# Kernel optimization log

Hardware: AMD Instinct MI355X
Metric: run time of the kernel (lower is better)

Reference implementation:

```python
import jax, jax.numpy as jnp
import numpy as np

WIDTH = 4096
NUM_HEADS = 8
BLOCK_W = WIDTH // NUM_HEADS


def _block_diag_linear(x, w, b):
    # x: [n, width] -> [n, h, bw]; w: [h, bw, bw]; b: [h, bw]
    n = x.shape[0]
    xh = x.reshape(n, NUM_HEADS, BLOCK_W)
    y = jnp.einsum('nhi,hij->nhj', xh, w) + b
    return y.reshape(n, WIDTH)


def setup_inputs() -> dict:
    key = jax.random.key(0)
    ks = jax.random.split(key, 7)
    n = 8192
    x = jax.random.normal(ks[0], (n, WIDTH), dtype=jnp.float32)
    s = jnp.sort(jax.random.randint(ks[1], (n,), 0, 8, dtype=jnp.int32))
    # a_param init: uniform on ring radii [0.9, 0.999], softplus-inverse transform
    eps = 1e-8
    u = jax.random.uniform(ks[2], (WIDTH,), minval=0.9**2 + eps, maxval=0.999**2 + eps)
    t = 0.5 * jnp.log(u)
    a_param = jnp.log(jnp.exp(-t) - 1.0).astype(jnp.float32)
    std = 1.0 / np.sqrt(BLOCK_W)
    ig_w = std * jax.random.normal(ks[3], (NUM_HEADS, BLOCK_W, BLOCK_W), dtype=jnp.float32)
    ig_b = jnp.zeros((NUM_HEADS, BLOCK_W), dtype=jnp.float32)
    ag_w = std * jax.random.normal(ks[4], (NUM_HEADS, BLOCK_W, BLOCK_W), dtype=jnp.float32)
    ag_b = jnp.zeros((NUM_HEADS, BLOCK_W), dtype=jnp.float32)
    return {'x': x, 's': s, 'a_param': a_param, 'ig_w': ig_w, 'ig_b': ig_b,
            'ag_w': ag_w, 'ag_b': ag_b}


def reference(x, s, a_param, ig_w, ig_b, ag_w, ag_b):
    n, k = x.shape
    # reset mask: True at position 0 and wherever segment id changes
    reset = jnp.concatenate([jnp.ones((1,), dtype=bool), s[1:] != s[:-1]])
    gate_x = jax.nn.sigmoid(_block_diag_linear(x, ig_w, ig_b))
    gate_a = jax.nn.sigmoid(_block_diag_linear(x, ag_w, ag_b))
    log_a = -8.0 * gate_a * jax.nn.softplus(a_param)  # [n, k]
    a = jnp.exp(log_a)
    a_square = jnp.exp(2.0 * log_a)
    multiplier = jnp.sqrt(1.0 - a_square)
    multiplier = jnp.where(reset[:, None], 1.0, multiplier)
    normalized_x = x * gate_x * multiplier
    # linear recurrence h[t] = a[t] * h[t-1] + normalized_x[t] via parallel scan
    def combine(e1, e2):
        a1, b1 = e1
        a2, b2 = e2
        return (a1 * a2, a2 * b1 + b2)
    _, out = jax.lax.associative_scan(combine, (a, normalized_x), axis=0)
    return out
```

## Files before the change

kernel.cpp:

```cpp
#include <hip/hip_runtime.h>
#include <hip/hip_bf16.h>
#include <stdint.h>

#define WIDTH 4096
#define NROWS 8192
#define NHEADS 8
#define BW 512
#define CS 128
#define NCHUNK (NROWS/CS)

typedef short bf16x8 __attribute__((ext_vector_type(8)));
typedef float f32x4 __attribute__((ext_vector_type(4)));

__device__ __forceinline__ uint32_t rne_bf16(float f) {
  uint32_t u = __float_as_uint(f);
  return (u + 0x7fffu + ((u >> 16) & 1u)) >> 16;
}
__device__ __forceinline__ uint32_t pack2(float lo, float hi) {
  return rne_bf16(lo) | (rne_bf16(hi) << 16);
}
__device__ __forceinline__ float bf16_to_f32(uint32_t bits) {
  return __uint_as_float(bits << 16);
}

__device__ __forceinline__ void gload_lds16(const void* g, void* l) {
  __builtin_amdgcn_global_load_lds(
      (const __attribute__((address_space(1))) void*)g,
      (__attribute__((address_space(3))) void*)l, 16, 0, 0);
}

__global__ void prep_xbf16(const float* __restrict__ x, uint16_t* __restrict__ xb) {
  size_t i = ((size_t)blockIdx.x * 256 + threadIdx.x) * 8;
  float4 f0 = *reinterpret_cast<const float4*>(x + i);
  float4 f1 = *reinterpret_cast<const float4*>(x + i + 4);
  uint4 v;
  v.x = pack2(f0.x, f0.y); v.y = pack2(f0.z, f0.w);
  v.z = pack2(f1.x, f1.y); v.w = pack2(f1.z, f1.w);
  *reinterpret_cast<uint4*>(xb + i) = v;
}

__global__ void prep_weights(const float* __restrict__ ig_w,
                             const float* __restrict__ ag_w,
                             uint16_t* __restrict__ wt) {
  __shared__ float tile[32][33];
  int j0 = blockIdx.x * 32;
  int i0 = blockIdx.y * 32;
  int m  = blockIdx.z;
  const float* src = ((m >> 3) ? ag_w : ig_w) + (size_t)(m & 7) * BW * BW;
  int tx = threadIdx.x & 31, ty = threadIdx.x >> 5;
  #pragma unroll
  for (int k = 0; k < 4; k++) {
    int i = i0 + ty + 8 * k;
    tile[ty + 8 * k][tx] = src[(size_t)i * BW + (j0 + tx)];
  }
  __syncthreads();
  #pragma unroll
  for (int k = 0; k < 4; k++) {
    int j = j0 + ty + 8 * k;
    wt[((size_t)m * BW + j) * BW + (i0 + tx)] = (uint16_t)rne_bf16(tile[tx][ty + 8 * k]);
  }
}

__global__ void prep_misc(const float* __restrict__ a_param, float* __restrict__ cvec) {
  int i = blockIdx.x * 256 + threadIdx.x;
  if (i < WIDTH) {
    float x = a_param[i];
    float sp = (x > 15.f) ? x : log1pf(expf(x));
    cvec[i] = 8.f * sp;
  }
}

#define BM 128
#define BN 128
#define BK 64

__global__ __launch_bounds__(256, 2)
void gates_gemm(const uint16_t* __restrict__ xb,
                const int* __restrict__ s,
                const uint16_t* __restrict__ wt,
                const float* __restrict__ ig_b,
                const float* __restrict__ ag_b,
                const float* __restrict__ cvec,
                uint16_t* __restrict__ la_buf,
                uint16_t* __restrict__ nx_buf,
                float* __restrict__ cA,
                float* __restrict__ cB) {
  __shared__ __align__(16) unsigned char smem[49152];
  __shared__ unsigned char resetm[BM];

  const int b = blockIdx.x;
  const int orig = (b & 7) * 256 + (b >> 3);
  const int h  = orig >> 8;
  const int rem = orig & 255;
  const int mt = rem >> 2;
  const int nt = rem & 3;
  const int m0 = mt * BM;
  const int j0 = nt * BN;

  const int tid = threadIdx.x;
  const int lane = tid & 63;
  const int w = tid >> 6;
  const int wr = w >> 1;
  const int wc = w & 1;
  const int lrow = lane & 15;
  const int lkg  = lane >> 4;

  if (tid < BM) {
    int n = m0 + tid;
    resetm[tid] = (n == 0) || (s[n] != s[n - 1]);
  }

  const char* xb_src[4];
  #pragma unroll
  for (int i = 0; i < 4; i++) {
    int o = (4 * w + i) * 1024 + (lane << 4);
    int row = o >> 7;
    int c = (o & 127) ^ ((row & 7) << 4);
    xb_src[i] = (const char*)xb + ((size_t)(m0 + row) * WIDTH + h * BW) * 2 + c;
  }
  const char* w_src[8];
  #pragma unroll
  for (int i = 0; i < 8; i++) {
    int o = (8 * w + i) * 1024 + (lane << 4);
    int g = o >> 14;
    int jl = (o >> 7) & 127;
    int c = (o & 127) ^ ((jl & 7) << 4);
    w_src[i] = (const char*)wt + ((size_t)((g * 8 + h) * BW + (j0 + jl)) * BW) * 2 + c;
  }

  f32x4 acc[2][4][4];
  #pragma unroll
  for (int g = 0; g < 2; g++)
    #pragma unroll
    for (int mf = 0; mf < 4; mf++)
      #pragma unroll
      for (int nf = 0; nf < 4; nf++)
        acc[g][mf][nf] = (f32x4){0.f, 0.f, 0.f, 0.f};

  for (int kt = 0; kt < 8; kt++) {
    __syncthreads();
    #pragma unroll
    for (int i = 0; i < 4; i++)
      gload_lds16(xb_src[i] + kt * 128, smem + (4 * w + i) * 1024);
    #pragma unroll
    for (int i = 0; i < 8; i++)
      gload_lds16(w_src[i] + kt * 128, smem + 16384 + (8 * w + i) * 1024);
    __syncthreads();
    #pragma unroll
    for (int ks = 0; ks < 2; ks++) {
      bf16x8 af[4];
      #pragma unroll
      for (int mf = 0; mf < 4; mf++) {
        int row = wr * 64 + 16 * mf + lrow;
        uint32_t addr = (uint32_t)((row << 7) + ks * 64 + lkg * 16);
        addr ^= (uint32_t)((row & 7) << 4);
        af[mf] = *reinterpret_cast<const bf16x8*>(smem + addr);
      }
      #pragma unroll
      for (int g = 0; g < 2; g++) {
        #pragma unroll
        for (int nf = 0; nf < 4; nf++) {
          int j = wc * 64 + 16 * nf + lrow;
          uint32_t addr = (uint32_t)(16384 + (g << 14) + (j << 7) + ks * 64 + lkg * 16);
          addr ^= (uint32_t)((j & 7) << 4);
          bf16x8 bfr = *reinterpret_cast<const bf16x8*>(smem + addr);
          #pragma unroll
          for (int mf = 0; mf < 4; mf++) {
            acc[g][mf][nf] = __builtin_amdgcn_mfma_f32_16x16x32_bf16(
                af[mf], bfr, acc[g][mf][nf], 0, 0, 0);
          }
        }
      }
    }
  }

  __syncthreads();
  float* smf = (float*)smem;

  #pragma unroll
  for (int nf = 0; nf < 4; nf++) {
    int j = j0 + wc * 64 + 16 * nf + lrow;
    int jj = h * BW + j;
    float igb = ig_b[jj], agb = ag_b[jj], cv = cvec[jj];
    float segA[4], segB[4];
    #pragma unroll
    for (int mf = 0; mf < 4; mf++) {
      float A = 1.f, B = 0.f;
      int nbase = m0 + wr * 64 + 16 * mf + 4 * lkg;
      #pragma unroll
      for (int r = 0; r < 4; r++) {
        int n = nbase + r;
        size_t o = (size_t)n * WIDTH + jj;
        float yig = acc[0][mf][nf][r] + igb;
        float yag = acc[1][mf][nf][r] + agb;
        float gx = __builtin_amdgcn_rcpf(1.f + __expf(-yig));
        float ga = __builtin_amdgcn_rcpf(1.f + __expf(-yag));
        float la = -ga * cv;
        uint32_t la_bits = rne_bf16(la);
        float la_r = bf16_to_f32(la_bits);
        float a = __expf(la_r);
        float mult = resetm[n - m0] ? 1.f
                     : __builtin_amdgcn_sqrtf(fmaxf(1.f - a * a, 0.f));
        float xv = bf16_to_f32((uint32_t)xb[o]);
        float nx = xv * gx * mult;
        uint32_t nx_bits = rne_bf16(nx);
        float nx_r = bf16_to_f32(nx_bits);
        la_buf[o] = (uint16_t)la_bits;
        nx_buf[o] = (uint16_t)nx_bits;
        A *= a;
        B = fmaf(a, B, nx_r);
      }
      segA[mf] = A; segB[mf] = B;
    }
    #pragma unroll
    for (int mf = 0; mf < 4; mf++) {
      float A = segA[mf], B = segB[mf];
      #pragma unroll
      for (int d = 16; d <= 32; d <<= 1) {
        float pA = __shfl_xor(A, d, 64);
        float pB = __shfl_xor(B, d, 64);
        bool up = (lane & d) != 0;
        B = up ? fmaf(A, pB, B) : fmaf(pA, B, pB);
        A *= pA;
      }
      segA[mf] = A; segB[mf] = B;
    }
    float colA = segA[0], colB = segB[0];
    #pragma unroll
    for (int mf = 1; mf < 4; mf++) {
      colB = fmaf(segA[mf], colB, segB[mf]);
      colA *= segA[mf];
    }
    if (lkg == 0) {
      int clocal = wc * 64 + 16 * nf + lrow;
      smf[wr * 128 + clocal] = colA;
      smf[256 + wr * 128 + clocal] = colB;
    }
  }
  __syncthreads();
  if (tid < BN) {
    float A0 = smf[tid],        B0 = smf[256 + tid];
    float A1 = smf[128 + tid],  B1 = smf[384 + tid];
    float Af = A0 * A1;
    float Bf = fmaf(A1, B0, B1);
    int jj = h * BW + j0 + tid;
    cA[mt * WIDTH + jj] = Af;
    cB[mt * WIDTH + jj] = Bf;
  }
}

__global__ void scan_prefix(const float* __restrict__ cA, const float* __restrict__ cB,
                            float* __restrict__ prefix) {
  int c = blockIdx.x * 256 + threadIdx.x;
  float hcur = 0.f;
  for (int i0 = 0; i0 < NCHUNK; i0 += 8) {
    float av[8], bv[8];
    #pragma unroll
    for (int e = 0; e < 8; e++) { av[e] = cA[(i0 + e) * WIDTH + c]; bv[e] = cB[(i0 + e) * WIDTH + c]; }
    #pragma unroll
    for (int e = 0; e < 8; e++) { prefix[(i0 + e) * WIDTH + c] = hcur; hcur = av[e] * hcur + bv[e]; }
  }
}

__global__ void scan_apply(const uint16_t* __restrict__ la_buf,
                           const uint16_t* __restrict__ nx_buf,
                           const float* __restrict__ prefix,
                           float* __restrict__ out) {
  int chunk = blockIdx.x;
  int c0 = (blockIdx.y * 256 + threadIdx.x) * 4;
  size_t base = (size_t)chunk * CS * WIDTH + c0;
  float h[4];
  #pragma unroll
  for (int q = 0; q < 4; q++) h[q] = prefix[chunk * WIDTH + c0 + q];
  for (int rb = 0; rb < CS; rb += 4) {
    ushort4 lav[4], nxv[4];
    #pragma unroll
    for (int e = 0; e < 4; e++) {
      size_t o = base + (size_t)(rb + e) * WIDTH;
      lav[e] = *reinterpret_cast<const ushort4*>(la_buf + o);
      nxv[e] = *reinterpret_cast<const ushort4*>(nx_buf + o);
    }
    #pragma unroll
    for (int e = 0; e < 4; e++) {
      float4 ov;
      h[0] = fmaf(__expf(bf16_to_f32(lav[e].x)), h[0], bf16_to_f32(nxv[e].x)); ov.x = h[0];
      h[1] = fmaf(__expf(bf16_to_f32(lav[e].y)), h[1], bf16_to_f32(nxv[e].y)); ov.y = h[1];
      h[2] = fmaf(__expf(bf16_to_f32(lav[e].z)), h[2], bf16_to_f32(nxv[e].z)); ov.z = h[2];
      h[3] = fmaf(__expf(bf16_to_f32(lav[e].w)), h[3], bf16_to_f32(nxv[e].w)); ov.w = h[3];
      *reinterpret_cast<float4*>(out + base + (size_t)(rb + e) * WIDTH) = ov;
    }
  }
}

extern "C" void kernel_launch(void* const* d_in, const int* in_sizes, int n_in,
                              void* d_out, int out_size, void* d_ws, size_t ws_size,
                              hipStream_t stream) {
  const float* x       = (const float*)d_in[0];
  const int*   s       = (const int*)d_in[1];
  const float* a_param = (const float*)d_in[2];
  const float* ig_w    = (const float*)d_in[3];
  const float* ig_b    = (const float*)d_in[4];
  const float* ag_w    = (const float*)d_in[5];
  const float* ag_b    = (const float*)d_in[6];
  float* out = (float*)d_out;
  char* ws = (char*)d_ws;

  uint16_t* la_buf = (uint16_t*)ws;
  uint16_t* nx_buf = (uint16_t*)(ws + 67108864);
  uint16_t* wt     = (uint16_t*)(ws + 134217728);
  uint16_t* xb     = (uint16_t*)(ws + 142606336);
  float*    cvec   = (float*)(ws + 209715200);
  float*    cA     = (float*)(ws + 209731584);
  float*    cB     = (float*)(ws + 210780160);
  float*    prefix = (float*)(ws + 211828736);

  prep_xbf16<<<dim3(16384), 256, 0, stream>>>(x, xb);
  prep_weights<<<dim3(16, 16, 16), 256, 0, stream>>>(ig_w, ag_w, wt);
  prep_misc<<<dim3(16), 256, 0, stream>>>(a_param, cvec);
  gates_gemm<<<dim3(2048), 256, 0, stream>>>(xb, s, wt, ig_b, ag_b, cvec,
                                             la_buf, nx_buf, cA, cB);
  scan_prefix<<<dim3(16), 256, 0, stream>>>(cA, cB, prefix);
  scan_apply<<<dim3(NCHUNK, 4), 256, 0, stream>>>(la_buf, nx_buf, prefix, out);
}
```

Baseline: 240.2 us.

## Double-buffer GEMM LDS with 256-row tiles and pack la/nx into one buffer

Enlarges the gates GEMM tile to 256 rows with 512 threads and double-buffers the LDS k-tiles, so the next tile's global-to-LDS loads overlap the current MFMA work and one barrier per k-step is removed. The weight tile is now loaded once per 256 rows instead of once per 128, halving weight traffic. The log-a and normalized-x bf16 outputs are packed into a single 32-bit buffer so scan_apply does one vector load per element instead of two. The 128KB of dynamic LDS allows at most one block per CU despite launch_bounds asking for two, which lowers occupancy.

```diff
diff --git a/kernel.cpp b/kernel.cpp
--- a/kernel.cpp
+++ b/kernel.cpp
@@ -70,28 +70,27 @@
   }
 }
 
-#define BM 128
+#define BM 256
 #define BN 128
 #define BK 64
 
-__global__ __launch_bounds__(256, 2)
+__global__ __launch_bounds__(512, 2)
 void gates_gemm(const uint16_t* __restrict__ xb,
                 const int* __restrict__ s,
                 const uint16_t* __restrict__ wt,
                 const float* __restrict__ ig_b,
                 const float* __restrict__ ag_b,
                 const float* __restrict__ cvec,
-                uint16_t* __restrict__ la_buf,
-                uint16_t* __restrict__ nx_buf,
+                uint32_t* __restrict__ lanx,
                 float* __restrict__ cA,
                 float* __restrict__ cB) {
-  __shared__ __align__(16) unsigned char smem[49152];
+  extern __shared__ __align__(16) unsigned char dsm[];
   __shared__ unsigned char resetm[BM];
 
   const int b = blockIdx.x;
-  const int orig = (b & 7) * 256 + (b >> 3);
-  const int h  = orig >> 8;
-  const int rem = orig & 255;
+  const int orig = (b & 7) * 128 + (b >> 3);
+  const int h  = orig >> 7;
+  const int rem = orig & 127;
   const int mt = rem >> 2;
   const int nt = rem & 3;
   const int m0 = mt * BM;
@@ -116,16 +115,16 @@
     int o = (4 * w + i) * 1024 + (lane << 4);
     int row = o >> 7;
     int c = (o & 127) ^ ((row & 7) << 4);
-    xb_src[i] = (const char*)xb + ((size_t)(m0 + row) * WIDTH + h * BW) * 2 + c;
-  }
-  const char* w_src[8];
-  #pragma unroll
-  for (int i = 0; i < 8; i++) {
-    int o = (8 * w + i) * 1024 + (lane << 4);
+    xb_src[i] = (const char*)xb + (size_t)(m0 + row) * (WIDTH * 2) + h * (BW * 2) + c;
+  }
+  const char* w_src[4];
+  #pragma unroll
+  for (int i = 0; i < 4; i++) {
+    int o = (4 * w + i) * 1024 + (lane << 4);
     int g = o >> 14;
     int jl = (o >> 7) & 127;
     int c = (o & 127) ^ ((jl & 7) << 4);
-    w_src[i] = (const char*)wt + ((size_t)((g * 8 + h) * BW + (j0 + jl)) * BW) * 2 + c;
+    w_src[i] = (const char*)wt + ((size_t)((g * 8 + h) * BW + (j0 + jl))) * (BW * 2) + c;
   }
 
   f32x4 acc[2][4][4];
@@ -137,33 +136,43 @@
       for (int nf = 0; nf < 4; nf++)
         acc[g][mf][nf] = (f32x4){0.f, 0.f, 0.f, 0.f};
 
+  #pragma unroll
+  for (int i = 0; i < 4; i++)
+    gload_lds16(xb_src[i], dsm + (4 * w + i) * 1024);
+  #pragma unroll
+  for (int i = 0; i < 4; i++)
+    gload_lds16(w_src[i], dsm + 32768 + (4 * w + i) * 1024);
+  __syncthreads();
+
   for (int kt = 0; kt < 8; kt++) {
-    __syncthreads();
-    #pragma unroll
-    for (int i = 0; i < 4; i++)
-      gload_lds16(xb_src[i] + kt * 128, smem + (4 * w + i) * 1024);
-    #pragma unroll
-    for (int i = 0; i < 8; i++)
-      gload_lds16(w_src[i] + kt * 128, smem + 16384 + (8 * w + i) * 1024);
-    __syncthreads();
+    const uint32_t cbase = (uint32_t)(kt & 1) << 16;
+    if (kt < 7) {
+      const uint32_t nbase = cbase ^ 65536u;
+      #pragma unroll
+      for (int i = 0; i < 4; i++)
+        gload_lds16(xb_src[i] + (kt + 1) * 128, dsm + nbase + (4 * w + i) * 1024);
+      #pragma unroll
+      for (int i = 0; i < 4; i++)
+        gload_lds16(w_src[i] + (kt + 1) * 128, dsm + nbase + 32768 + (4 * w + i) * 1024);
+    }
     #pragma unroll
     for (int ks = 0; ks < 2; ks++) {
       bf16x8 af[4];
       #pragma unroll
       for (int mf = 0; mf < 4; mf++) {
         int row = wr * 64 + 16 * mf + lrow;
-        uint32_t addr = (uint32_t)((row << 7) + ks * 64 + lkg * 16);
+        uint32_t addr = cbase + (uint32_t)((row << 7) + ks * 64 + lkg * 16);
         addr ^= (uint32_t)((row & 7) << 4);
-        af[mf] = *reinterpret_cast<const bf16x8*>(smem + addr);
+        af[mf] = *reinterpret_cast<const bf16x8*>(dsm + addr);
       }
       #pragma unroll
       for (int g = 0; g < 2; g++) {
         #pragma unroll
         for (int nf = 0; nf < 4; nf++) {
           int j = wc * 64 + 16 * nf + lrow;
-          uint32_t addr = (uint32_t)(16384 + (g << 14) + (j << 7) + ks * 64 + lkg * 16);
+          uint32_t addr = cbase + (uint32_t)(32768 + (g << 14) + (j << 7) + ks * 64 + lkg * 16);
           addr ^= (uint32_t)((j & 7) << 4);
-          bf16x8 bfr = *reinterpret_cast<const bf16x8*>(smem + addr);
+          bf16x8 bfr = *reinterpret_cast<const bf16x8*>(dsm + addr);
           #pragma unroll
           for (int mf = 0; mf < 4; mf++) {
             acc[g][mf][nf] = __builtin_amdgcn_mfma_f32_16x16x32_bf16(
@@ -172,10 +181,10 @@
         }
       }
     }
-  }
-
-  __syncthreads();
-  float* smf = (float*)smem;
+    __syncthreads();
+  }
+
+  float* smf = (float*)dsm;
 
   #pragma unroll
   for (int nf = 0; nf < 4; nf++) {
@@ -205,8 +214,7 @@
         float nx = xv * gx * mult;
         uint32_t nx_bits = rne_bf16(nx);
         float nx_r = bf16_to_f32(nx_bits);
-        la_buf[o] = (uint16_t)la_bits;
-        nx_buf[o] = (uint16_t)nx_bits;
+        lanx[o] = la_bits | (nx_bits << 16);
         A *= a;
         B = fmaf(a, B, nx_r);
       }
@@ -234,18 +242,22 @@
     if (lkg == 0) {
       int clocal = wc * 64 + 16 * nf + lrow;
       smf[wr * 128 + clocal] = colA;
-      smf[256 + wr * 128 + clocal] = colB;
+      smf[512 + wr * 128 + clocal] = colB;
     }
   }
   __syncthreads();
-  if (tid < BN) {
-    float A0 = smf[tid],        B0 = smf[256 + tid];
-    float A1 = smf[128 + tid],  B1 = smf[384 + tid];
+  if (tid < 256) {
+    int half = tid >> 7;
+    int cl = tid & 127;
+    int base = half * 2;
+    float A0 = smf[base * 128 + cl],       B0 = smf[512 + base * 128 + cl];
+    float A1 = smf[(base + 1) * 128 + cl], B1 = smf[512 + (base + 1) * 128 + cl];
     float Af = A0 * A1;
     float Bf = fmaf(A1, B0, B1);
-    int jj = h * BW + j0 + tid;
-    cA[mt * WIDTH + jj] = Af;
-    cB[mt * WIDTH + jj] = Bf;
+    int ct = mt * 2 + half;
+    int jj = h * BW + j0 + cl;
+    cA[ct * WIDTH + jj] = Af;
+    cB[ct * WIDTH + jj] = Bf;
   }
 }
 
@@ -262,8 +274,7 @@
   }
 }
 
-__global__ void scan_apply(const uint16_t* __restrict__ la_buf,
-                           const uint16_t* __restrict__ nx_buf,
+__global__ void scan_apply(const uint32_t* __restrict__ lanx,
                            const float* __restrict__ prefix,
                            float* __restrict__ out) {
   int chunk = blockIdx.x;
@@ -273,20 +284,17 @@
   #pragma unroll
   for (int q = 0; q < 4; q++) h[q] = prefix[chunk * WIDTH + c0 + q];
   for (int rb = 0; rb < CS; rb += 4) {
-    ushort4 lav[4], nxv[4];
-    #pragma unroll
-    for (int e = 0; e < 4; e++) {
-      size_t o = base + (size_t)(rb + e) * WIDTH;
-      lav[e] = *reinterpret_cast<const ushort4*>(la_buf + o);
-      nxv[e] = *reinterpret_cast<const ushort4*>(nx_buf + o);
-    }
+    uint4 v[4];
+    #pragma unroll
+    for (int e = 0; e < 4; e++)
+      v[e] = *reinterpret_cast<const uint4*>(lanx + base + (size_t)(rb + e) * WIDTH);
     #pragma unroll
     for (int e = 0; e < 4; e++) {
       float4 ov;
-      h[0] = fmaf(__expf(bf16_to_f32(lav[e].x)), h[0], bf16_to_f32(nxv[e].x)); ov.x = h[0];
-      h[1] = fmaf(__expf(bf16_to_f32(lav[e].y)), h[1], bf16_to_f32(nxv[e].y)); ov.y = h[1];
-      h[2] = fmaf(__expf(bf16_to_f32(lav[e].z)), h[2], bf16_to_f32(nxv[e].z)); ov.z = h[2];
-      h[3] = fmaf(__expf(bf16_to_f32(lav[e].w)), h[3], bf16_to_f32(nxv[e].w)); ov.w = h[3];
+      h[0] = fmaf(__expf(bf16_to_f32(v[e].x & 0xffffu)), h[0], bf16_to_f32(v[e].x >> 16)); ov.x = h[0];
+      h[1] = fmaf(__expf(bf16_to_f32(v[e].y & 0xffffu)), h[1], bf16_to_f32(v[e].y >> 16)); ov.y = h[1];
+      h[2] = fmaf(__expf(bf16_to_f32(v[e].z & 0xffffu)), h[2], bf16_to_f32(v[e].z >> 16)); ov.z = h[2];
+      h[3] = fmaf(__expf(bf16_to_f32(v[e].w & 0xffffu)), h[3], bf16_to_f32(v[e].w >> 16)); ov.w = h[3];
       *reinterpret_cast<float4*>(out + base + (size_t)(rb + e) * WIDTH) = ov;
     }
   }
@@ -305,8 +313,7 @@
   float* out = (float*)d_out;
   char* ws = (char*)d_ws;
 
-  uint16_t* la_buf = (uint16_t*)ws;
-  uint16_t* nx_buf = (uint16_t*)(ws + 67108864);
+  uint32_t* lanx   = (uint32_t*)ws;
   uint16_t* wt     = (uint16_t*)(ws + 134217728);
   uint16_t* xb     = (uint16_t*)(ws + 142606336);
   float*    cvec   = (float*)(ws + 209715200);
@@ -317,8 +324,8 @@
   prep_xbf16<<<dim3(16384), 256, 0, stream>>>(x, xb);
   prep_weights<<<dim3(16, 16, 16), 256, 0, stream>>>(ig_w, ag_w, wt);
   prep_misc<<<dim3(16), 256, 0, stream>>>(a_param, cvec);
-  gates_gemm<<<dim3(2048), 256, 0, stream>>>(xb, s, wt, ig_b, ag_b, cvec,
-                                             la_buf, nx_buf, cA, cB);
+  gates_gemm<<<dim3(1024), dim3(512), 131072, stream>>>(xb, s, wt, ig_b, ag_b, cvec,
+                                                        lanx, cA, cB);
   scan_prefix<<<dim3(16), 256, 0, stream>>>(cA, cB, prefix);
-  scan_apply<<<dim3(NCHUNK, 4), 256, 0, stream>>>(la_buf, nx_buf, prefix, out);
-}
+  scan_apply<<<dim3(NCHUNK, 4), 256, 0, stream>>>(lanx, prefix, out);
+}
```

Result: faster. 219.5 us (-8.6%).
